# Kernel optimization log

Measured on AMD Instinct MI355X. Metric: run time of the kernel, lower is better.

The kernel has to match this reference:

```python
import jax, jax.numpy as jnp
import numpy as np

HEADS = 8
EPS = 1e-5

def _conv2d(x, w, b):
    # x: (b,c,h,w), w: (out_c,in_c,3,3), padding=1 (SAME)
    y = jax.lax.conv_general_dilated(x, w, (1, 1), ((1, 1), (1, 1)),
                                     dimension_numbers=('NCHW', 'OIHW', 'NCHW'))
    return y + b[None, :, None, None]

def _mcl(x, cw, cb, pw):
    # MultichannelLinear: conv then per-channel pointwise matmul over the h (feature) dim
    y = _conv2d(x, cw, cb)                      # (b,c,in_f,w)
    return jnp.einsum('bchw,cfh->bcfw', y, pw)  # (b,c,out_f,w)

def _ln(x, g, b):
    # MultichannelLayerNorm over the feature (h) axis with per-channel affine
    mu = x.mean(axis=2, keepdims=True)
    var = x.var(axis=2, keepdims=True)
    xn = (x - mu) * jax.lax.rsqrt(var + EPS)
    return xn * g[None, :, :, None] + b[None, :, :, None]

def _rope(t):
    # lucidrains RotaryEmbedding.rotate_queries_or_keys, interleaved pairs; t: (...,w,d)
    d = t.shape[-1]
    w = t.shape[-2]
    inv = 1.0 / (10000.0 ** (jnp.arange(0, d, 2, dtype=jnp.float32) / d))
    ang = jnp.arange(w, dtype=jnp.float32)[:, None] * inv[None, :]   # (w, d/2)
    cos = jnp.repeat(jnp.cos(ang), 2, axis=-1)
    sin = jnp.repeat(jnp.sin(ang), 2, axis=-1)
    t2 = t.reshape(t.shape[:-1] + (d // 2, 2))
    rot = jnp.stack([-t2[..., 1], t2[..., 0]], axis=-1).reshape(t.shape)
    return t * cos + rot * sin

def _split_heads(y, nh):
    b, c, f, w = y.shape
    return y.transpose(0, 1, 3, 2).reshape(b, c, w, nh, f // nh).transpose(0, 1, 3, 2, 4)  # (b,c,nh,w,dh)

def _forward(x, embed_cw, embed_cb, embed_pw, norm1_g, norm1_b,
             q_cw, q_cb, q_pw, k_cw, k_cb, k_pw, v_cw, v_cb, v_pw,
             o_cw, o_cb, o_pw, norm2_g, norm2_b,
             ffn1_cw, ffn1_cb, ffn1_pw, ffn2_cw, ffn2_cb, ffn2_pw):
    b, c_in, hdim, w = x.shape
    h0 = _mcl(x, embed_cw, embed_cb, embed_pw)          # (b,c,feat,w)
    # --- multichannel multihead attention with inline RoPE ---
    xn = _ln(h0, norm1_g, norm1_b)
    q = _rope(_split_heads(_mcl(xn, q_cw, q_cb, q_pw), HEADS))   # (b,c,nh,w,dh)
    k = _rope(_split_heads(_mcl(xn, k_cw, k_cb, k_pw), HEADS))
    v = _split_heads(_mcl(xn, v_cw, v_cb, v_pw), HEADS)
    qk = jnp.einsum('bchqd,bchkd->bchqk', q, k) / jnp.sqrt(jnp.float32(hdim))  # scale by sqrt(h), per source
    a = jnp.einsum('bchqk,bchkd->bchqd', jax.nn.softmax(qk, axis=-1), v)
    bb, cc, nh, ww, dh = a.shape
    a = a.transpose(0, 1, 3, 2, 4).reshape(bb, cc, ww, nh * dh).transpose(0, 1, 3, 2)  # (b,c,feat,w)
    z = _mcl(a, o_cw, o_cb, o_pw)
    h = h0 + z
    # --- squared-ReLU FFN ---
    y = _mcl(_ln(h, norm2_g, norm2_b), ffn1_cw, ffn1_cb, ffn1_pw)
    y = jnp.maximum(y, 0.0) ** 2
    z = _mcl(y, ffn2_cw, ffn2_cb, ffn2_pw)
    h = h + z
    return jnp.concatenate([x, h], axis=1)  # (b, c_in+c_out, feat, w)

def setup_inputs() -> dict:
    key = jax.random.key(0)
    ks = jax.random.split(key, 32)
    C_IN, C, F, W, B, EXP = 8, 4, 1024, 512, 4, 4

    def p(k, shape, fan):
        return jax.random.normal(k, shape, dtype=jnp.float32) * (1.0 / np.sqrt(fan))

    inp = {
        'x': jax.random.normal(ks[0], (B, C_IN, F, W), dtype=jnp.float32),
        'embed_cw': p(ks[1], (C, C_IN, 3, 3), C_IN * 9), 'embed_cb': p(ks[2], (C,), C_IN * 9),
        'embed_pw': p(ks[3], (C, F, F), F),
        'norm1_g': jnp.ones((C, F), jnp.float32), 'norm1_b': jnp.zeros((C, F), jnp.float32),
        'q_cw': p(ks[4], (C, C, 3, 3), C * 9), 'q_cb': p(ks[5], (C,), C * 9), 'q_pw': p(ks[6], (C, F, F), F),
        'k_cw': p(ks[7], (C, C, 3, 3), C * 9), 'k_cb': p(ks[8], (C,), C * 9), 'k_pw': p(ks[9], (C, F, F), F),
        'v_cw': p(ks[10], (C, C, 3, 3), C * 9), 'v_cb': p(ks[11], (C,), C * 9), 'v_pw': p(ks[12], (C, F, F), F),
        'o_cw': p(ks[13], (C, C, 3, 3), C * 9), 'o_cb': p(ks[14], (C,), C * 9), 'o_pw': p(ks[15], (C, F, F), F),
        'norm2_g': jnp.ones((C, F), jnp.float32), 'norm2_b': jnp.zeros((C, F), jnp.float32),
        'ffn1_cw': p(ks[16], (C, C, 3, 3), C * 9), 'ffn1_cb': p(ks[17], (C,), C * 9),
        'ffn1_pw': p(ks[18], (C, F * EXP, F), F),
        'ffn2_cw': p(ks[19], (C, C, 3, 3), C * 9), 'ffn2_cb': p(ks[20], (C,), C * 9),
        'ffn2_pw': p(ks[21], (C, F, F * EXP), F * EXP),
    }
    return inp

def reference(x, embed_cw, embed_cb, embed_pw, norm1_g, norm1_b,
              q_cw, q_cb, q_pw, k_cw, k_cb, k_pw, v_cw, v_cb, v_pw,
              o_cw, o_cb, o_pw, norm2_g, norm2_b,
              ffn1_cw, ffn1_cb, ffn1_pw, ffn2_cw, ffn2_cb, ffn2_pw):
    return _forward(x, embed_cw, embed_cb, embed_pw, norm1_g, norm1_b,
                    q_cw, q_cb, q_pw, k_cw, k_cb, k_pw, v_cw, v_cb, v_pw,
                    o_cw, o_cb, o_pw, norm2_g, norm2_b,
                    ffn1_cw, ffn1_cb, ffn1_pw, ffn2_cw, ffn2_cb, ffn2_pw)
```

## Files before the change

### kernel.cpp

```cpp
#include <hip/hip_runtime.h>

typedef __attribute__((ext_vector_type(8))) short short8;
typedef __attribute__((ext_vector_type(4))) float f32x4;
typedef unsigned int uint;
typedef unsigned short ushort;

#define PLF 524288

__device__ __forceinline__ ushort f2bf(float f) {
  uint u = __float_as_uint(f);
  u += 0x7FFF + ((u >> 16) & 1);
  return (ushort)(u >> 16);
}
__device__ __forceinline__ float bf2f(ushort h) {
  return __uint_as_float(((uint)h) << 16);
}
__device__ __forceinline__ int swzf(int r) { return ((r & 3) ^ ((r >> 2) & 3)); }

#define GLOAD16(gp, lp)                                          \
  __builtin_amdgcn_global_load_lds(                              \
      (const __attribute__((address_space(1))) void*)(gp),       \
      (__attribute__((address_space(3))) void*)(lp), 16, 0, 0)

template <int CDT, int BETA, int RELU2, int MFAST, int BCVT, int ROPE>
__global__ __launch_bounds__(256) void mm_kernel(
    const void* __restrict__ Av, const void* __restrict__ Bv, void* __restrict__ Cv,
    int K, int lda, int ldb, int ldc,
    int aDiv, int aMod, long long aS1, long long aS2,
    int bDiv, int bMod, long long bS1, long long bS2,
    int cDiv, int cMod, long long cS1, long long cS2, float alpha)
{
  __shared__ char lds[49152];
  const int nx = gridDim.x, ny = gridDim.y;
  const int nwg = nx * ny * (int)gridDim.z;
  const int o = ((int)blockIdx.z * ny + blockIdx.y) * nx + blockIdx.x;
  const int qd = nwg >> 3, rm = nwg & 7, xcd = o & 7, rot = o >> 3;
  const int wflat = (xcd < rm ? xcd * (qd + 1) : rm * (qd + 1) + (xcd - rm) * qd) + rot;
  int bx, by, bz;
  if (MFAST) { by = wflat % ny; int t2 = wflat / ny; bx = t2 % nx; bz = t2 / nx; }
  else       { bx = wflat % nx; int t2 = wflat / nx; by = t2 % ny; bz = t2 / ny; }
  const int tid = threadIdx.x;
  const long long aOff = (long long)(bz / aDiv) * aS1 + (long long)(bz % aMod) * aS2;
  const long long bOff = (long long)(bz / bDiv) * bS1 + (long long)(bz % bMod) * bS2;
  const long long cOff = (long long)(bz / cDiv) * cS1 + (long long)(bz % cMod) * cS2;
  const int m0 = by * 128, n0 = bx * 128;
  const int lane = tid & 63, wid = tid >> 6;
  const int MOFF = (wid >> 1) * 64, NOFF = (wid & 1) * 64;
  const int u = lane & 15, g = lane >> 4;
  const int sr0 = tid >> 2, sslot = tid & 3;
  const ushort* Ap = (const ushort*)Av + aOff;
  const ushort* Bp = (const ushort*)Bv + bOff;
  const float*  Bf = (const float*)Bv + bOff;

#define STAGE(buf, kt)                                                         \
  {                                                                            \
    _Pragma("unroll")                                                          \
    for (int half = 0; half < 2; ++half) {                                     \
      const int r = sr0 + 64 * half;                                           \
      const int ss = sslot ^ swzf(r);                                          \
      GLOAD16(Ap + (long long)(m0 + r) * lda + (kt) + ss * 8,                  \
              &lds[(buf) * 16384] + wid * 1024 + half * 4096);                 \
      if (BCVT == 0) {                                                         \
        GLOAD16(Bp + (long long)(n0 + r) * ldb + (kt) + ss * 8,                \
                &lds[(buf) * 16384 + 8192] + wid * 1024 + half * 4096);        \
      } else {                                                                 \
        const float* srcB = Bf + (long long)(n0 + r) * ldb + (kt) + ss * 8;    \
        float4 x0 = *(const float4*)srcB;                                      \
        float4 x1 = *(const float4*)(srcB + 4);                                \
        short8 h;                                                              \
        h[0] = (short)f2bf(x0.x); h[1] = (short)f2bf(x0.y);                    \
        h[2] = (short)f2bf(x0.z); h[3] = (short)f2bf(x0.w);                    \
        h[4] = (short)f2bf(x1.x); h[5] = (short)f2bf(x1.y);                    \
        h[6] = (short)f2bf(x1.z); h[7] = (short)f2bf(x1.w);                    \
        *(short8*)(&lds[(buf) * 16384 + 8192] + r * 64 + sslot * 16) = h;      \
      }                                                                        \
    }                                                                          \
  }

  f32x4 acc[4][4];
#pragma unroll
  for (int i = 0; i < 4; ++i)
#pragma unroll
    for (int j = 0; j < 4; ++j) acc[i][j] = (f32x4){0.f, 0.f, 0.f, 0.f};

  const int T = K >> 5;
  STAGE(0, 0);
  if (T > 1) STAGE(1, 32);
  int rb = 0, sb = 2;
  for (int t = 0; t < T; ++t) {
    if (BCVT == 0) {
      if (t + 1 < T) { asm volatile("s_waitcnt vmcnt(4)" ::: "memory"); }
      else           { asm volatile("s_waitcnt vmcnt(0)" ::: "memory"); }
    } else {
      asm volatile("s_waitcnt vmcnt(0) lgkmcnt(0)" ::: "memory");
    }
    __builtin_amdgcn_s_barrier();
    __builtin_amdgcn_sched_barrier(0);
    asm volatile("" ::: "memory");
    if (t + 2 < T) STAGE(sb, (t + 2) * 32);
    const char* Abuf = &lds[rb * 16384];
    const char* Bbuf = &lds[rb * 16384 + 8192];
    short8 af[4], bfr[4];
#pragma unroll
    for (int mi = 0; mi < 4; ++mi) {
      const int r = MOFF + mi * 16 + u;
      af[mi] = *(const short8*)(Abuf + r * 64 + ((g ^ swzf(r)) * 16));
    }
#pragma unroll
    for (int ni = 0; ni < 4; ++ni) {
      const int r = NOFF + ni * 16 + u;
      bfr[ni] = *(const short8*)(Bbuf + r * 64 + ((g ^ swzf(r)) * 16));
    }
#pragma unroll
    for (int mi = 0; mi < 4; ++mi)
#pragma unroll
      for (int ni = 0; ni < 4; ++ni)
        acc[mi][ni] = __builtin_amdgcn_mfma_f32_16x16x32_bf16(af[mi], bfr[ni], acc[mi][ni], 0, 0, 0);
    rb = (rb == 2) ? 0 : rb + 1;
    sb = (sb == 2) ? 0 : sb + 1;
  }
#undef STAGE

#pragma unroll
  for (int mi = 0; mi < 4; ++mi)
#pragma unroll
    for (int ni = 0; ni < 4; ++ni)
#pragma unroll
      for (int q = 0; q < 4; ++q) {
        const int row = m0 + MOFF + mi * 16 + g * 4 + q;
        const int col = n0 + NOFF + ni * 16 + u;
        float v = acc[mi][ni][q] * alpha;
        if (CDT == 0) {
          float* cp = (float*)Cv + cOff + (long long)row * ldc + col;
          if (BETA) v += *cp;
          *cp = v;
        } else {
          if (ROPE) {
            const int j = (col & 127) >> 1;
            const float infr = __expf((float)j * (-9.210340371976184f / 64.f));
            float sn, cs;
            __sincosf((float)row * infr, &sn, &cs);
            const float part = __shfl_xor(v, 1);
            v = (col & 1) ? fmaf(part, sn, v * cs) : fmaf(-part, sn, v * cs);
          }
          if (RELU2) { v = fmaxf(v, 0.f); v = v * v; }
          ((ushort*)Cv)[cOff + (long long)row * ldc + col] = f2bf(v);
        }
      }
}

__global__ __launch_bounds__(256) void fattn_kernel(
    const ushort* __restrict__ Qg, const ushort* __restrict__ Kg,
    const ushort* __restrict__ Vg, ushort* __restrict__ Og)
{
  __shared__ char lds[73728];
  const int hb = blockIdx.y, pl = hb >> 3, h = hb & 7;
  const int q0 = blockIdx.x * 64;
  const int tid = threadIdx.x, lane = tid & 63, wv = tid >> 6;
  const int u = lane & 15, g = lane >> 4;
  const ushort* Qh = Qg + (size_t)pl * PLF + h * 128;
  const ushort* Kh = Kg + (size_t)pl * PLF + h * 128;
  const ushort* Vh = Vg + (size_t)pl * PLF + (size_t)(h * 128) * 512;
  ushort* Oh = Og + (size_t)pl * PLF + h * 128;

  short8 qf[4];
  const int qrow = q0 + wv * 16 + u;
#pragma unroll
  for (int dc = 0; dc < 4; ++dc)
    qf[dc] = *(const short8*)(Qh + (size_t)qrow * 1024 + dc * 32 + g * 8);

#define STAGE_KV(buf, kt)                                                     \
  {                                                                           \
    _Pragma("unroll")                                                         \
    for (int it = 0; it < 4; ++it) {                                          \
      const int off = tid * 16 + it * 4096;                                   \
      const int krow = off >> 8, kslot = (off >> 4) & 15;                     \
      GLOAD16(Kh + (size_t)((kt) * 64 + krow) * 1024 +                        \
                  ((kslot ^ ((krow & 7) << 1)) * 8),                          \
              &lds[(buf) * 16384] + off);                                     \
      const int vrow = off >> 7, vslot = (off >> 4) & 7;                      \
      GLOAD16(Vh + (size_t)vrow * 512 + (kt) * 64 + ((vslot ^ (vrow & 7)) * 8), \
              &lds[32768 + (buf) * 16384] + off);                             \
    }                                                                         \
  }

  f32x4 oacc[8];
#pragma unroll
  for (int i = 0; i < 8; ++i) oacc[i] = (f32x4){0.f, 0.f, 0.f, 0.f};
  float m_run = -3.0e38f, l_run = 0.f;

  STAGE_KV(0, 0);
  asm volatile("s_waitcnt vmcnt(0)" ::: "memory");
  __syncthreads();
  int cur = 0;
  for (int kt = 0; kt < 8; ++kt) {
    if (kt + 1 < 8) STAGE_KV(cur ^ 1, kt + 1);
    f32x4 sacc[4];
#pragma unroll
    for (int kn = 0; kn < 4; ++kn) sacc[kn] = (f32x4){0.f, 0.f, 0.f, 0.f};
    __builtin_amdgcn_s_setprio(1);
#pragma unroll
    for (int kn = 0; kn < 4; ++kn) {
      const int r = kn * 16 + u;
      const char* kb = &lds[cur * 16384] + r * 256;
#pragma unroll
      for (int dc = 0; dc < 4; ++dc) {
        short8 kf = *(const short8*)(kb + (((dc * 4 + g) ^ ((u & 7) << 1)) * 16));
        sacc[kn] = __builtin_amdgcn_mfma_f32_16x16x32_bf16(kf, qf[dc], sacc[kn], 0, 0, 0);
      }
    }
    __builtin_amdgcn_s_setprio(0);
    float pm = -3.0e38f;
#pragma unroll
    for (int kn = 0; kn < 4; ++kn)
#pragma unroll
      for (int r = 0; r < 4; ++r) {
        sacc[kn][r] *= 0.03125f;
        pm = fmaxf(pm, sacc[kn][r]);
      }
    pm = fmaxf(pm, __shfl_xor(pm, 16));
    pm = fmaxf(pm, __shfl_xor(pm, 32));
    const float m_new = fmaxf(m_run, pm);
    const float es = __expf(m_run - m_new);
    float psum = 0.f;
    uint pw[4][2];
#pragma unroll
    for (int kn = 0; kn < 4; ++kn) {
      float p0 = __expf(sacc[kn][0] - m_new);
      float p1 = __expf(sacc[kn][1] - m_new);
      float p2 = __expf(sacc[kn][2] - m_new);
      float p3 = __expf(sacc[kn][3] - m_new);
      psum += (p0 + p1) + (p2 + p3);
      pw[kn][0] = (uint)f2bf(p0) | ((uint)f2bf(p1) << 16);
      pw[kn][1] = (uint)f2bf(p2) | ((uint)f2bf(p3) << 16);
    }
    psum += __shfl_xor(psum, 16);
    psum += __shfl_xor(psum, 32);
    l_run = l_run * es + psum;
    m_run = m_new;
    char* pb = &lds[65536 + wv * 2048] + u * 128 + (g & 1) * 8;
#pragma unroll
    for (int kn = 0; kn < 4; ++kn)
      *(uint2*)(pb + (((2 * kn + (g >> 1)) ^ (u & 7)) * 16)) =
          make_uint2(pw[kn][0], pw[kn][1]);
    float es_o[4];
#pragma unroll
    for (int r = 0; r < 4; ++r) es_o[r] = __shfl(es, g * 4 + r);
#pragma unroll
    for (int nd = 0; nd < 8; ++nd)
#pragma unroll
      for (int r = 0; r < 4; ++r) oacc[nd][r] *= es_o[r];
    const char* prd = &lds[65536 + wv * 2048] + u * 128;
    short8 pf[2];
#pragma unroll
    for (int kc = 0; kc < 2; ++kc)
      pf[kc] = *(const short8*)(prd + (((kc * 4 + g) ^ (u & 7)) * 16));
    __builtin_amdgcn_s_setprio(1);
#pragma unroll
    for (int nd = 0; nd < 8; ++nd) {
      const int vr = nd * 16 + u;
      const char* vb = &lds[32768 + cur * 16384] + vr * 128;
#pragma unroll
      for (int kc = 0; kc < 2; ++kc) {
        short8 vf = *(const short8*)(vb + (((kc * 4 + g) ^ (u & 7)) * 16));
        oacc[nd] = __builtin_amdgcn_mfma_f32_16x16x32_bf16(pf[kc], vf, oacc[nd], 0, 0, 0);
      }
    }
    __builtin_amdgcn_s_setprio(0);
    asm volatile("s_waitcnt vmcnt(0)" ::: "memory");
    __syncthreads();
    cur ^= 1;
  }
#undef STAGE_KV
  const float inv_l = 1.f / l_run;
  float inv_o[4];
#pragma unroll
  for (int r = 0; r < 4; ++r) inv_o[r] = __shfl(inv_l, g * 4 + r);
#pragma unroll
  for (int nd = 0; nd < 8; ++nd)
#pragma unroll
    for (int r = 0; r < 4; ++r) {
      const int row = q0 + wv * 16 + g * 4 + r;
      Oh[(size_t)row * 1024 + nd * 16 + u] = f2bf(oacc[nd][r] * inv_o[r]);
    }
}

__global__ __launch_bounds__(256) void cvt_kernel(
    const float4* __restrict__ s, short8* __restrict__ d)
{
  const int i = blockIdx.x * 256 + threadIdx.x;
  const float4 a = s[2 * i], b = s[2 * i + 1];
  short8 h;
  h[0] = (short)f2bf(a.x); h[1] = (short)f2bf(a.y);
  h[2] = (short)f2bf(a.z); h[3] = (short)f2bf(a.w);
  h[4] = (short)f2bf(b.x); h[5] = (short)f2bf(b.y);
  h[6] = (short)f2bf(b.z); h[7] = (short)f2bf(b.w);
  d[i] = h;
}

template <int CIN>
__global__ __launch_bounds__(256) void conv4c_kernel(
    const ushort* __restrict__ in, const float* __restrict__ wt,
    const float* __restrict__ bias, ushort* __restrict__ outp, int log2F)
{
  const int idx = blockIdx.x * 256 + threadIdx.x;
  const int F8m = (1 << (log2F - 3)) - 1;
  const int f8 = idx & F8m;
  const int wp2 = (idx >> (log2F - 3)) & 255;
  const int bb = idx >> (log2F + 5);
  const int w = wp2 * 2;
  const int f0 = f8 << 3;
  float acc[2][4][8];
#pragma unroll
  for (int co = 0; co < 4; ++co) {
    const float bv = bias[co];
#pragma unroll
    for (int j = 0; j < 8; ++j) { acc[0][co][j] = bv; acc[1][co][j] = bv; }
  }
  const bool lok = f8 > 0, rok = f8 < F8m;
#pragma unroll
  for (int ci = 0; ci < CIN; ++ci) {
    const ushort* base = in + (((size_t)(bb * CIN + ci)) << (log2F + 9));
#pragma unroll
    for (int rr = 0; rr < 4; ++rr) {
      const int wr = w - 1 + rr;
      if (wr < 0 || wr > 511) continue;
      const ushort* rp = base + ((size_t)wr << log2F) + f0;
      const short8 cen = *(const short8*)rp;
      float xv[10];
      xv[0] = lok ? bf2f(rp[-1]) : 0.f;
#pragma unroll
      for (int j = 0; j < 8; ++j) xv[j + 1] = bf2f((ushort)cen[j]);
      xv[9] = rok ? bf2f(rp[8]) : 0.f;
#pragma unroll
      for (int co = 0; co < 4; ++co) {
        const float* wp = wt + (co * CIN + ci) * 9;
        if (rr <= 2) {
          const float k0 = wp[rr], k1 = wp[3 + rr], k2 = wp[6 + rr];
#pragma unroll
          for (int j = 0; j < 8; ++j)
            acc[0][co][j] += k0 * xv[j] + k1 * xv[j + 1] + k2 * xv[j + 2];
        }
        if (rr >= 1) {
          const float k0 = wp[rr - 1], k1 = wp[2 + rr], k2 = wp[5 + rr];
#pragma unroll
          for (int j = 0; j < 8; ++j)
            acc[1][co][j] += k0 * xv[j] + k1 * xv[j + 1] + k2 * xv[j + 2];
        }
      }
    }
  }
#pragma unroll
  for (int wo = 0; wo < 2; ++wo)
#pragma unroll
    for (int co = 0; co < 4; ++co) {
      short8 o;
#pragma unroll
      for (int j = 0; j < 8; ++j) o[j] = (short)f2bf(acc[wo][co][j]);
      *(short8*)(outp + (((size_t)(bb * 4 + co)) << (log2F + 9)) +
                 ((size_t)(w + wo) << log2F) + f0) = o;
    }
}

__global__ __launch_bounds__(256) void conv12c_kernel(
    const ushort* __restrict__ in,
    const float* __restrict__ wq, const float* __restrict__ wk, const float* __restrict__ wv,
    const float* __restrict__ bq, const float* __restrict__ bk, const float* __restrict__ bv,
    ushort* __restrict__ outp, int nPl)
{
  const int idx = blockIdx.x * 256 + threadIdx.x;
  const int f8 = idx & 127;
  const int w = (idx >> 7) & 511;
  const int bb = idx >> 16;
  const int f0 = f8 << 3;
  const float* wsel[3] = {wq, wk, wv};
  float acc[12][8];
#pragma unroll
  for (int co = 0; co < 4; ++co) {
    const float b0 = bq[co], b1 = bk[co], b2 = bv[co];
#pragma unroll
    for (int j = 0; j < 8; ++j) {
      acc[co][j] = b0; acc[4 + co][j] = b1; acc[8 + co][j] = b2;
    }
  }
  const bool lok = f8 > 0, rok = f8 < 127;
#pragma unroll
  for (int ci = 0; ci < 4; ++ci) {
    const ushort* base = in + (((size_t)(bb * 4 + ci)) << 19);
#pragma unroll
    for (int dxw = 0; dxw < 3; ++dxw) {
      const int w2 = w + dxw - 1;
      if (w2 < 0 || w2 > 511) continue;
      const ushort* rp = base + ((size_t)w2 << 10) + f0;
      const short8 cen = *(const short8*)rp;
      float xv[10];
      xv[0] = lok ? bf2f(rp[-1]) : 0.f;
#pragma unroll
      for (int j = 0; j < 8; ++j) xv[j + 1] = bf2f((ushort)cen[j]);
      xv[9] = rok ? bf2f(rp[8]) : 0.f;
#pragma unroll
      for (int pj = 0; pj < 3; ++pj)
#pragma unroll
        for (int co = 0; co < 4; ++co) {
          const float* wp = wsel[pj] + (co * 4 + ci) * 9;
          const float k0 = wp[dxw], k1 = wp[3 + dxw], k2 = wp[6 + dxw];
#pragma unroll
          for (int j = 0; j < 8; ++j)
            acc[pj * 4 + co][j] += k0 * xv[j] + k1 * xv[j + 1] + k2 * xv[j + 2];
        }
    }
  }
#pragma unroll
  for (int pj = 0; pj < 3; ++pj)
#pragma unroll
    for (int co = 0; co < 4; ++co) {
      short8 o;
#pragma unroll
      for (int j = 0; j < 8; ++j) o[j] = (short)f2bf(acc[pj * 4 + co][j]);
      *(short8*)(outp + (((size_t)(pj * nPl + bb * 4 + co)) << 19) +
                 ((size_t)w << 10) + f0) = o;
    }
}

__global__ __launch_bounds__(256) void ln_kernel(
    const float* __restrict__ H, const float* __restrict__ gam,
    const float* __restrict__ bet, ushort* __restrict__ XN)
{
  const int wid = threadIdx.x >> 6, lane = threadIdx.x & 63;
  const int row = blockIdx.x * 4 + wid;
  const int c = (row >> 9) & 3;
  const float* xp = H + (size_t)row * 1024;
  float4 v[4];
  float s = 0.f, q = 0.f;
#pragma unroll
  for (int p = 0; p < 4; ++p) {
    v[p] = *(const float4*)(xp + p * 256 + lane * 4);
    s += v[p].x + v[p].y + v[p].z + v[p].w;
    q += v[p].x * v[p].x + v[p].y * v[p].y + v[p].z * v[p].z + v[p].w * v[p].w;
  }
#pragma unroll
  for (int o = 32; o > 0; o >>= 1) { s += __shfl_xor(s, o); q += __shfl_xor(q, o); }
  const float mu = s * (1.f / 1024.f);
  const float var = q * (1.f / 1024.f) - mu * mu;
  const float rs = rsqrtf(var + 1e-5f);
  ushort* op = XN + (size_t)row * 1024;
  const float* gp = gam + c * 1024;
  const float* bp = bet + c * 1024;
#pragma unroll
  for (int p = 0; p < 4; ++p) {
    const int f = p * 256 + lane * 4;
    float4 g4 = *(const float4*)(gp + f);
    float4 b4 = *(const float4*)(bp + f);
    ushort4 o4;
    o4.x = f2bf((v[p].x - mu) * rs * g4.x + b4.x);
    o4.y = f2bf((v[p].y - mu) * rs * g4.y + b4.y);
    o4.z = f2bf((v[p].z - mu) * rs * g4.z + b4.z);
    o4.w = f2bf((v[p].w - mu) * rs * g4.w + b4.w);
    *(ushort4*)(op + f) = o4;
  }
}

__global__ __launch_bounds__(256) void tin_kernel(
    const float* __restrict__ x, ushort* __restrict__ XT,
    float* __restrict__ outp, int planeOff)
{
  __shared__ float t[32][33];
  const int f0 = blockIdx.x * 32, w0 = blockIdx.y * 32;
  const int z = blockIdx.z;
  const int tx = threadIdx.x & 31, ty = threadIdx.x >> 5;
  const int gpl = planeOff + z;
  const int b = gpl >> 3, ch = gpl & 7;
  const float* src = x + (size_t)gpl * PLF;
  float* dst0 = outp + (size_t)(b * 12 + ch) * PLF;
#pragma unroll
  for (int r = 0; r < 32; r += 8) {
    const size_t off = (size_t)(f0 + r + ty) * 512 + w0 + tx;
    const float v = src[off];
    t[r + ty][tx] = v;
    dst0[off] = v;
  }
  __syncthreads();
  ushort* dst = XT + (size_t)z * PLF;
#pragma unroll
  for (int r = 0; r < 32; r += 8) dst[(size_t)(w0 + r + ty) * 1024 + f0 + tx] = f2bf(t[tx][r + ty]);
}

__global__ __launch_bounds__(256) void tout_kernel(
    const float* __restrict__ H, float* __restrict__ out, int b0)
{
  __shared__ float t[32][33];
  const int w0 = blockIdx.x * 32, f0 = blockIdx.y * 32;
  const int p = blockIdx.z;
  const int b = b0 + (p >> 2), c = p & 3;
  const int tx = threadIdx.x & 31, ty = threadIdx.x >> 5;
  const float* src = H + (size_t)p * PLF;
#pragma unroll
  for (int r = 0; r < 32; r += 8) t[r + ty][tx] = src[(size_t)(w0 + r + ty) * 1024 + f0 + tx];
  __syncthreads();
  float* dst = out + (size_t)(b * 12 + 8 + c) * PLF;
#pragma unroll
  for (int r = 0; r < 32; r += 8) dst[(size_t)(f0 + r + ty) * 512 + w0 + tx] = t[tx][r + ty];
}

extern "C" void kernel_launch(void* const* d_in, const int* in_sizes, int n_in,
                              void* d_out, int out_size, void* d_ws, size_t ws_size,
                              hipStream_t stream)
{
  const float* x        = (const float*)d_in[0];
  const float* embed_cw = (const float*)d_in[1];
  const float* embed_cb = (const float*)d_in[2];
  const float* embed_pw = (const float*)d_in[3];
  const float* n1g      = (const float*)d_in[4];
  const float* n1b      = (const float*)d_in[5];
  const float* q_cw     = (const float*)d_in[6];
  const float* q_cb     = (const float*)d_in[7];
  const float* q_pw     = (const float*)d_in[8];
  const float* k_cw     = (const float*)d_in[9];
  const float* k_cb     = (const float*)d_in[10];
  const float* k_pw     = (const float*)d_in[11];
  const float* v_cw     = (const float*)d_in[12];
  const float* v_cb     = (const float*)d_in[13];
  const float* v_pw     = (const float*)d_in[14];
  const float* o_cw     = (const float*)d_in[15];
  const float* o_cb     = (const float*)d_in[16];
  const float* o_pw     = (const float*)d_in[17];
  const float* n2g      = (const float*)d_in[18];
  const float* n2b      = (const float*)d_in[19];
  const float* f1_cw    = (const float*)d_in[20];
  const float* f1_cb    = (const float*)d_in[21];
  const float* f1_pw    = (const float*)d_in[22];
  const float* f2_cw    = (const float*)d_in[23];
  const float* f2_cb    = (const float*)d_in[24];
  const float* f2_pw    = (const float*)d_in[25];
  float* out = (float*)d_out;

  const size_t perB = 50331648ull;
  const int N = (ws_size >= 4 * perB) ? 4 : (ws_size >= 2 * perB) ? 2 : 1;
  const int nP = 4 * N;

  char* base = (char*)d_ws;
  float*  Hf = (float*)base;
  ushort* XT = (ushort*)(base + (size_t)N * 8388608);
  ushort* XN = (ushort*)((char*)XT + (size_t)N * 8388608);
  ushort* Qb = (ushort*)((char*)XN + (size_t)N * 4194304);
  ushort* Kb = (ushort*)((char*)Qb + (size_t)N * 4194304);
  ushort* CT = (ushort*)((char*)Kb + (size_t)N * 4194304);
  ushort* Vb = (ushort*)((char*)CT + (size_t)N * 4194304);
  ushort* SfPb = (ushort*)((char*)Vb + (size_t)N * 4194304);
  ushort* CT3 = SfPb;
  ushort* W8  = SfPb;
  ushort* WQK = XT;
  ushort* MID = XT;
  ushort* f1w = Vb;
  ushort* F2C = Vb;
  ushort* f2w = XT;

  const long long W1 = 1048576;
  const long long W4 = 4194304;
  const long long M1 = 2097152;
  const long long CH3 = (long long)nP * PLF;
  const int GCc1 = N * 128;
  const int GCc4 = N * 512;
  const int GC12 = N * 256;

  for (int b0 = 0; b0 < 4; b0 += N) {
    tin_kernel<<<dim3(32, 16, 8 * N), 256, 0, stream>>>(x, XT, out, b0 * 8);
    conv4c_kernel<8><<<GCc1, 256, 0, stream>>>(XT, embed_cw, embed_cb, CT, 10);
    cvt_kernel<<<2048, 256, 0, stream>>>((const float4*)embed_pw, (short8*)W8);
    mm_kernel<0, 0, 0, 1, 0, 0><<<dim3(8, 4, nP), 256, 0, stream>>>(
        CT, W8, Hf, 1024, 1024, 1024, 1024,
        1, 1, PLF, 0, 4, 4, 0, W1, 1, 1, PLF, 0, 1.f);
    ln_kernel<<<nP * 128, 256, 0, stream>>>(Hf, n1g, n1b, XN);
    conv12c_kernel<<<GC12, 256, 0, stream>>>(XN, q_cw, k_cw, v_cw,
                                             q_cb, k_cb, v_cb, CT3, nP);
    if (N >= 2) {
      cvt_kernel<<<2048, 256, 0, stream>>>((const float4*)q_pw, (short8*)WQK);
      cvt_kernel<<<2048, 256, 0, stream>>>((const float4*)k_pw, (short8*)(WQK) + 524288);
      mm_kernel<1, 0, 0, 1, 0, 1><<<dim3(8, 4, 2 * nP), 256, 0, stream>>>(
          CT3, WQK, Qb, 1024, 1024, 1024, 1024,
          1, 1, PLF, 0, nP, 4, 4 * W1, W1, 1, 1, PLF, 0, 1.f);
    } else {
      mm_kernel<1, 0, 0, 1, 1, 1><<<dim3(8, 4, nP), 256, 0, stream>>>(
          CT3, q_pw, Qb, 1024, 1024, 1024, 1024,
          1, 1, PLF, 0, 4, 4, 0, W1, 1, 1, PLF, 0, 1.f);
      mm_kernel<1, 0, 0, 1, 1, 1><<<dim3(8, 4, nP), 256, 0, stream>>>(
          CT3 + CH3, k_pw, Kb, 1024, 1024, 1024, 1024,
          1, 1, PLF, 0, 4, 4, 0, W1, 1, 1, PLF, 0, 1.f);
    }
    cvt_kernel<<<2048, 256, 0, stream>>>((const float4*)v_pw, (short8*)W8);
    mm_kernel<1, 0, 0, 0, 0, 0><<<dim3(4, 8, nP), 256, 0, stream>>>(
        W8, CT3 + 2 * CH3, Vb, 1024, 1024, 1024, 512,
        4, 4, 0, W1, 1, 1, PLF, 0, 1, 1, PLF, 0, 1.f);
    fattn_kernel<<<dim3(8, nP * 8), 256, 0, stream>>>(Qb, Kb, Vb, Qb);
    conv4c_kernel<4><<<GCc1, 256, 0, stream>>>(Qb, o_cw, o_cb, CT, 10);
    cvt_kernel<<<2048, 256, 0, stream>>>((const float4*)o_pw, (short8*)W8);
    mm_kernel<0, 1, 0, 1, 0, 0><<<dim3(8, 4, nP), 256, 0, stream>>>(
        CT, W8, Hf, 1024, 1024, 1024, 1024,
        1, 1, PLF, 0, 4, 4, 0, W1, 1, 1, PLF, 0, 1.f);
    ln_kernel<<<nP * 128, 256, 0, stream>>>(Hf, n2g, n2b, XN);
    conv4c_kernel<4><<<GCc1, 256, 0, stream>>>(XN, f1_cw, f1_cb, CT, 10);
    if (N >= 2) {
      cvt_kernel<<<8192, 256, 0, stream>>>((const float4*)f1_pw, (short8*)f1w);
      mm_kernel<1, 0, 1, 1, 0, 0><<<dim3(32, 4, nP), 256, 0, stream>>>(
          CT, f1w, MID, 1024, 1024, 1024, 4096,
          1, 1, PLF, 0, 4, 4, 0, W4, 1, 1, M1, 0, 1.f);
    } else {
      mm_kernel<1, 0, 1, 1, 1, 0><<<dim3(32, 4, nP), 256, 0, stream>>>(
          CT, f1_pw, MID, 1024, 1024, 1024, 4096,
          1, 1, PLF, 0, 4, 4, 0, W4, 1, 1, M1, 0, 1.f);
    }
    conv4c_kernel<4><<<GCc4, 256, 0, stream>>>(MID, f2_cw, f2_cb, F2C, 12);
    if (N >= 2) {
      cvt_kernel<<<8192, 256, 0, stream>>>((const float4*)f2_pw, (short8*)f2w);
      mm_kernel<0, 1, 0, 1, 0, 0><<<dim3(8, 4, nP), 256, 0, stream>>>(
          F2C, f2w, Hf, 4096, 4096, 4096, 1024,
          1, 1, M1, 0, 4, 4, 0, W4, 1, 1, PLF, 0, 1.f);
    } else {
      mm_kernel<0, 1, 0, 1, 1, 0><<<dim3(8, 4, nP), 256, 0, stream>>>(
          F2C, f2_pw, Hf, 4096, 4096, 4096, 1024,
          1, 1, M1, 0, 4, 4, 0, W4, 1, 1, PLF, 0, 1.f);
    }
    tout_kernel<<<dim3(16, 32, nP), 256, 0, stream>>>(Hf, out, b0);
  }
}
```

Baseline: 659.7 us.

## Add 512-thread 128x256 GEMM kernel with triple-buffered LDS pipeline

Introduces mm2_kernel, a wider 128x256 output tile GEMM using 8 waves of 512 threads and three LDS stages with direct global-to-LDS loads. It replaces mm_kernel for all the N>=2 pointwise matmuls. The larger tile is meant to raise data reuse per byte loaded, and the deeper prefetch is meant to hide memory latency. The trade-off is half as many workgroups, more LDS per block and likely higher register pressure, which may lower occupancy and leave the grid less evenly filled.

```diff
diff --git a/kernel.cpp b/kernel.cpp
--- a/kernel.cpp
+++ b/kernel.cpp
@@ -21,6 +21,122 @@
   __builtin_amdgcn_global_load_lds(                              \
       (const __attribute__((address_space(1))) void*)(gp),       \
       (__attribute__((address_space(3))) void*)(lp), 16, 0, 0)
+
+template <int CDT, int BETA, int RELU2, int MFAST, int ROPE>
+__global__ __launch_bounds__(512) void mm2_kernel(
+    const ushort* __restrict__ Av, const ushort* __restrict__ Bv, void* __restrict__ Cv,
+    int K, int lda, int ldb, int ldc,
+    int aDiv, int aMod, long long aS1, long long aS2,
+    int bDiv, int bMod, long long bS1, long long bS2,
+    int cDiv, int cMod, long long cS1, long long cS2, float alpha)
+{
+  __shared__ char lds[73728];
+  const int nx = gridDim.x, ny = gridDim.y;
+  const int nwg = nx * ny * (int)gridDim.z;
+  const int o = ((int)blockIdx.z * ny + blockIdx.y) * nx + blockIdx.x;
+  const int qd = nwg >> 3, rm = nwg & 7, xcd = o & 7, rot = o >> 3;
+  const int wflat = (xcd < rm ? xcd * (qd + 1) : rm * (qd + 1) + (xcd - rm) * qd) + rot;
+  int bx, by, bz;
+  if (MFAST) { by = wflat % ny; int t2 = wflat / ny; bx = t2 % nx; bz = t2 / nx; }
+  else       { bx = wflat % nx; int t2 = wflat / nx; by = t2 % ny; bz = t2 / ny; }
+  const int tid = threadIdx.x;
+  const long long aOff = (long long)(bz / aDiv) * aS1 + (long long)(bz % aMod) * aS2;
+  const long long bOff = (long long)(bz / bDiv) * bS1 + (long long)(bz % bMod) * bS2;
+  const long long cOff = (long long)(bz / cDiv) * cS1 + (long long)(bz % cMod) * cS2;
+  const int m0 = by * 128, n0 = bx * 256;
+  const int lane = tid & 63, wid = tid >> 6;
+  const int MOFF = (wid >> 2) * 64, NOFF = (wid & 3) * 64;
+  const int u = lane & 15, g = lane >> 4;
+  const int sr0 = tid >> 2, sslot = tid & 3;
+  const ushort* Ap = Av + aOff;
+  const ushort* Bp = Bv + bOff;
+
+#define STAGE2(buf, kt)                                                        \
+  {                                                                            \
+    {                                                                          \
+      const int r = sr0;                                                       \
+      const int ss = sslot ^ swzf(r);                                          \
+      GLOAD16(Ap + (long long)(m0 + r) * lda + (kt) + ss * 8,                  \
+              &lds[(buf) * 24576] + tid * 16);                                 \
+    }                                                                          \
+    _Pragma("unroll")                                                          \
+    for (int half = 0; half < 2; ++half) {                                     \
+      const int r = sr0 + 128 * half;                                          \
+      const int ss = sslot ^ swzf(r);                                          \
+      GLOAD16(Bp + (long long)(n0 + r) * ldb + (kt) + ss * 8,                  \
+              &lds[(buf) * 24576 + 8192] + half * 8192 + tid * 16);            \
+    }                                                                          \
+  }
+
+  f32x4 acc[4][4];
+#pragma unroll
+  for (int i = 0; i < 4; ++i)
+#pragma unroll
+    for (int j = 0; j < 4; ++j) acc[i][j] = (f32x4){0.f, 0.f, 0.f, 0.f};
+
+  const int T = K >> 5;
+  STAGE2(0, 0);
+  if (T > 1) STAGE2(1, 32);
+  int rb = 0, sb = 2;
+  for (int t = 0; t < T; ++t) {
+    if (t + 1 < T) { asm volatile("s_waitcnt vmcnt(3)" ::: "memory"); }
+    else           { asm volatile("s_waitcnt vmcnt(0)" ::: "memory"); }
+    __builtin_amdgcn_s_barrier();
+    __builtin_amdgcn_sched_barrier(0);
+    asm volatile("" ::: "memory");
+    if (t + 2 < T) STAGE2(sb, (t + 2) * 32);
+    const char* Abuf = &lds[rb * 24576];
+    const char* Bbuf = &lds[rb * 24576 + 8192];
+    short8 af[4], bfr[4];
+#pragma unroll
+    for (int mi = 0; mi < 4; ++mi) {
+      const int r = MOFF + mi * 16 + u;
+      af[mi] = *(const short8*)(Abuf + r * 64 + ((g ^ swzf(r)) * 16));
+    }
+#pragma unroll
+    for (int ni = 0; ni < 4; ++ni) {
+      const int r = NOFF + ni * 16 + u;
+      bfr[ni] = *(const short8*)(Bbuf + r * 64 + ((g ^ swzf(r)) * 16));
+    }
+    __builtin_amdgcn_s_setprio(1);
+#pragma unroll
+    for (int mi = 0; mi < 4; ++mi)
+#pragma unroll
+      for (int ni = 0; ni < 4; ++ni)
+        acc[mi][ni] = __builtin_amdgcn_mfma_f32_16x16x32_bf16(af[mi], bfr[ni], acc[mi][ni], 0, 0, 0);
+    __builtin_amdgcn_s_setprio(0);
+    rb = (rb == 2) ? 0 : rb + 1;
+    sb = (sb == 2) ? 0 : sb + 1;
+  }
+#undef STAGE2
+
+#pragma unroll
+  for (int mi = 0; mi < 4; ++mi)
+#pragma unroll
+    for (int ni = 0; ni < 4; ++ni)
+#pragma unroll
+      for (int q = 0; q < 4; ++q) {
+        const int row = m0 + MOFF + mi * 16 + g * 4 + q;
+        const int col = n0 + NOFF + ni * 16 + u;
+        float v = acc[mi][ni][q] * alpha;
+        if (CDT == 0) {
+          float* cp = (float*)Cv + cOff + (long long)row * ldc + col;
+          if (BETA) v += *cp;
+          *cp = v;
+        } else {
+          if (ROPE) {
+            const int j = (col & 127) >> 1;
+            const float infr = __expf((float)j * (-9.210340371976184f / 64.f));
+            float sn, cs;
+            __sincosf((float)row * infr, &sn, &cs);
+            const float part = __shfl_xor(v, 1);
+            v = (col & 1) ? fmaf(part, sn, v * cs) : fmaf(-part, sn, v * cs);
+          }
+          if (RELU2) { v = fmaxf(v, 0.f); v = v * v; }
+          ((ushort*)Cv)[cOff + (long long)row * ldc + col] = f2bf(v);
+        }
+      }
+}
 
 template <int CDT, int BETA, int RELU2, int MFAST, int BCVT, int ROPE>
 __global__ __launch_bounds__(256) void mm_kernel(
@@ -567,7 +683,7 @@
     tin_kernel<<<dim3(32, 16, 8 * N), 256, 0, stream>>>(x, XT, out, b0 * 8);
     conv4c_kernel<8><<<GCc1, 256, 0, stream>>>(XT, embed_cw, embed_cb, CT, 10);
     cvt_kernel<<<2048, 256, 0, stream>>>((const float4*)embed_pw, (short8*)W8);
-    mm_kernel<0, 0, 0, 1, 0, 0><<<dim3(8, 4, nP), 256, 0, stream>>>(
+    mm2_kernel<0, 0, 0, 1, 0><<<dim3(4, 4, nP), 512, 0, stream>>>(
         CT, W8, Hf, 1024, 1024, 1024, 1024,
         1, 1, PLF, 0, 4, 4, 0, W1, 1, 1, PLF, 0, 1.f);
     ln_kernel<<<nP * 128, 256, 0, stream>>>(Hf, n1g, n1b, XN);
@@ -576,7 +692,7 @@
     if (N >= 2) {
       cvt_kernel<<<2048, 256, 0, stream>>>((const float4*)q_pw, (short8*)WQK);
       cvt_kernel<<<2048, 256, 0, stream>>>((const float4*)k_pw, (short8*)(WQK) + 524288);
-      mm_kernel<1, 0, 0, 1, 0, 1><<<dim3(8, 4, 2 * nP), 256, 0, stream>>>(
+      mm2_kernel<1, 0, 0, 1, 1><<<dim3(4, 4, 2 * nP), 512, 0, stream>>>(
           CT3, WQK, Qb, 1024, 1024, 1024, 1024,
           1, 1, PLF, 0, nP, 4, 4 * W1, W1, 1, 1, PLF, 0, 1.f);
     } else {
@@ -588,20 +704,20 @@
           1, 1, PLF, 0, 4, 4, 0, W1, 1, 1, PLF, 0, 1.f);
     }
     cvt_kernel<<<2048, 256, 0, stream>>>((const float4*)v_pw, (short8*)W8);
-    mm_kernel<1, 0, 0, 0, 0, 0><<<dim3(4, 8, nP), 256, 0, stream>>>(
+    mm2_kernel<1, 0, 0, 0, 0><<<dim3(2, 8, nP), 512, 0, stream>>>(
         W8, CT3 + 2 * CH3, Vb, 1024, 1024, 1024, 512,
         4, 4, 0, W1, 1, 1, PLF, 0, 1, 1, PLF, 0, 1.f);
     fattn_kernel<<<dim3(8, nP * 8), 256, 0, stream>>>(Qb, Kb, Vb, Qb);
     conv4c_kernel<4><<<GCc1, 256, 0, stream>>>(Qb, o_cw, o_cb, CT, 10);
     cvt_kernel<<<2048, 256, 0, stream>>>((const float4*)o_pw, (short8*)W8);
-    mm_kernel<0, 1, 0, 1, 0, 0><<<dim3(8, 4, nP), 256, 0, stream>>>(
+    mm2_kernel<0, 1, 0, 1, 0><<<dim3(4, 4, nP), 512, 0, stream>>>(
         CT, W8, Hf, 1024, 1024, 1024, 1024,
         1, 1, PLF, 0, 4, 4, 0, W1, 1, 1, PLF, 0, 1.f);
     ln_kernel<<<nP * 128, 256, 0, stream>>>(Hf, n2g, n2b, XN);
     conv4c_kernel<4><<<GCc1, 256, 0, stream>>>(XN, f1_cw, f1_cb, CT, 10);
     if (N >= 2) {
       cvt_kernel<<<8192, 256, 0, stream>>>((const float4*)f1_pw, (short8*)f1w);
-      mm_kernel<1, 0, 1, 1, 0, 0><<<dim3(32, 4, nP), 256, 0, stream>>>(
+      mm2_kernel<1, 0, 1, 1, 0><<<dim3(16, 4, nP), 512, 0, stream>>>(
           CT, f1w, MID, 1024, 1024, 1024, 4096,
           1, 1, PLF, 0, 4, 4, 0, W4, 1, 1, M1, 0, 1.f);
     } else {
@@ -612,7 +728,7 @@
     conv4c_kernel<4><<<GCc4, 256, 0, stream>>>(MID, f2_cw, f2_cb, F2C, 12);
     if (N >= 2) {
       cvt_kernel<<<8192, 256, 0, stream>>>((const float4*)f2_pw, (short8*)f2w);
-      mm_kernel<0, 1, 0, 1, 0, 0><<<dim3(8, 4, nP), 256, 0, stream>>>(
+      mm2_kernel<0, 1, 0, 1, 0><<<dim3(4, 4, nP), 512, 0, stream>>>(
           F2C, f2w, Hf, 4096, 4096, 4096, 1024,
           1, 1, M1, 0, 4, 4, 0, W4, 1, 1, PLF, 0, 1.f);
     } else {
```

New measurement: 646.9 us. Within noise of the previous version (-1.9%).
